# Optimization experiments

Hardware: AMD Instinct MI355X
Metric: run time of the kernel (lower is better)

The kernel has to match this reference:

```python
import jax, jax.numpy as jnp
import numpy as np

D_IN = 4096
D_OUT = 4096
B, S = 4, 2048


def setup_inputs() -> dict:
    key = jax.random.key(0)
    kx, kw, kb = jax.random.split(key, 3)
    x = jax.random.normal(kx, (B, S, D_IN), dtype=jnp.float32)
    # Simulate the quantized weight buffers exactly as QLinear.__init__ does:
    # per-tensor symmetric int8 quantization of a float weight.
    w_fp = jax.random.normal(kw, (D_OUT, D_IN), dtype=jnp.float32) * 0.02
    weight_scale = jnp.max(jnp.abs(w_fp)) / 127.0
    weight_int8 = jnp.round(w_fp / weight_scale).astype(jnp.int8)
    bias = jax.random.normal(kb, (D_OUT,), dtype=jnp.float32) * 0.01
    return {"x": x, "weight_int8": weight_int8, "weight_scale": weight_scale, "bias": bias}


def reference(x, weight_int8, weight_scale, bias):
    # Per-row (last-dim) fake int8 quant-dequant of activations.
    x_scales = jnp.max(jnp.abs(x), axis=-1, keepdims=True) / 127.0 + 1e-8
    xq = jnp.round(x / x_scales) * x_scales
    # Dequantize weight (per-tensor scale) and do the float GEMM.
    w = weight_int8.astype(x.dtype) * weight_scale  # [D_OUT, D_IN]
    y = jnp.einsum("bsd,od->bso", xq, w) + bias
    return y
```

## Files before the change

### kernel.cpp

```cpp
#include <hip/hip_runtime.h>
#include <stdint.h>

#define D_IN  4096
#define D_OUT 4096
#define M_TOT 8192

#define BM 128
#define BN 128
#define BK 64

using i32x4 = __attribute__((ext_vector_type(4))) int;

__global__ __launch_bounds__(256) void prep(
    const float* __restrict__ x, int8_t* __restrict__ xq,
    float* __restrict__ s_out,
    const int* __restrict__ w32, int8_t* __restrict__ w8)
{
    const int tid = threadIdx.x;
    const int b   = blockIdx.x;

    if (b < M_TOT) {
        __shared__ float wmax[4];
        const float* xr = x + (size_t)b * D_IN;

        float4 v[4];
        float m = 0.f;
#pragma unroll
        for (int c = 0; c < 4; ++c) {
            v[c] = ((const float4*)xr)[c * 256 + tid];
            m = fmaxf(m, fmaxf(fmaxf(fabsf(v[c].x), fabsf(v[c].y)),
                               fmaxf(fabsf(v[c].z), fabsf(v[c].w))));
        }
#pragma unroll
        for (int off = 1; off < 64; off <<= 1)
            m = fmaxf(m, __shfl_xor(m, off));
        if ((tid & 63) == 0) wmax[tid >> 6] = m;
        __syncthreads();
        m = fmaxf(fmaxf(wmax[0], wmax[1]), fmaxf(wmax[2], wmax[3]));

        const float s   = m / 127.0f + 1e-8f;
        const float inv = 1.0f / s;
        if (tid == 0) s_out[b] = s;

        int* q32 = (int*)(xq + (size_t)b * D_IN);
#pragma unroll
        for (int c = 0; c < 4; ++c) {
            int q0 = (int)rintf(v[c].x * inv);
            int q1 = (int)rintf(v[c].y * inv);
            int q2 = (int)rintf(v[c].z * inv);
            int q3 = (int)rintf(v[c].w * inv);
            q32[c * 256 + tid] = (q0 & 0xff) | ((q1 & 0xff) << 8) |
                                 ((q2 & 0xff) << 16) | ((q3 & 0xff) << 24);
        }
    } else {
        const int i = (b - M_TOT) * 256 + tid;
        int4 v = ((const int4*)w32)[i];
        ((int*)w8)[i] = (v.x & 0xff) | ((v.y & 0xff) << 8) |
                        ((v.z & 0xff) << 16) | ((v.w & 0xff) << 24);
    }
}

__device__ __forceinline__ void gload_lds16(const void* g, void* l) {
    __builtin_amdgcn_global_load_lds(
        (const __attribute__((address_space(1))) unsigned int*)(uintptr_t)g,
        (__attribute__((address_space(3))) unsigned int*)(uintptr_t)l,
        16, 0, 0);
}

__global__ __launch_bounds__(256) void gemm_i8(
    const int8_t* __restrict__ Aq, const int8_t* __restrict__ Wq,
    const float* __restrict__ srow, const float* __restrict__ wsc,
    const float* __restrict__ bias, float* __restrict__ Y)
{
    __shared__ int8_t lA[BM * BK];
    __shared__ int8_t lB[BN * BK];

    const int tid  = threadIdx.x;
    const int lane = tid & 63;
    const int wave = tid >> 6;

    const int b    = blockIdx.x;
    const int swz  = (b & 7) * 256 + (b >> 3);
    const int nbx  = D_OUT / BN;
    const int bn   = (swz % nbx) * BN;
    const int bm   = (swz / nbx) * BM;

    const int wr   = (wave >> 1) * 64;
    const int wc   = (wave & 1) * 64;

    i32x4 acc[4][4] = {};

    const int fr = lane & 15;
    const int fk = (lane >> 4) * 16;

    const int8_t* gA = Aq + (size_t)bm * D_IN;
    const int8_t* gW = Wq + (size_t)bn * D_IN;

    for (int kt = 0; kt < D_IN; kt += BK) {
#pragma unroll
        for (int j = 0; j < 2; ++j) {
            const int c  = j * 256 + tid;
            const int r  = c >> 2;
            const int ko = (c & 3) * 16;
            gload_lds16(gA + (size_t)r * D_IN + kt + ko, lA + c * 16);
            gload_lds16(gW + (size_t)r * D_IN + kt + ko, lB + c * 16);
        }
        __syncthreads();

        i32x4 a[4], bfr[4];
#pragma unroll
        for (int i = 0; i < 4; ++i) {
            a[i]   = *(const i32x4*)(lA + (wr + i * 16 + fr) * BK + fk);
            bfr[i] = *(const i32x4*)(lB + (wc + i * 16 + fr) * BK + fk);
        }
#pragma unroll
        for (int i = 0; i < 4; ++i)
#pragma unroll
            for (int j = 0; j < 4; ++j)
                acc[i][j] = __builtin_amdgcn_mfma_i32_16x16x64_i8(
                    a[i], bfr[j], acc[i][j], 0, 0, 0);
        __syncthreads();
    }

    const float ws = wsc[0];
    float bs[4];
#pragma unroll
    for (int j = 0; j < 4; ++j) bs[j] = bias[bn + wc + j * 16 + fr];

#pragma unroll
    for (int i = 0; i < 4; ++i) {
        const int m0 = bm + wr + i * 16 + (lane >> 4) * 4;
#pragma unroll
        for (int r = 0; r < 4; ++r) {
            const float sm = srow[m0 + r] * ws;
            float* yp = Y + (size_t)(m0 + r) * D_OUT + bn + wc + fr;
#pragma unroll
            for (int j = 0; j < 4; ++j)
                yp[j * 16] = (float)acc[i][j][r] * sm + bs[j];
        }
    }
}

extern "C" void kernel_launch(void* const* d_in, const int* in_sizes, int n_in,
                              void* d_out, int out_size, void* d_ws, size_t ws_size,
                              hipStream_t stream) {
    const float* x    = (const float*)d_in[0];
    const int*   w32  = (const int*)d_in[1];
    const float* wsc  = (const float*)d_in[2];
    const float* bias = (const float*)d_in[3];
    float* y = (float*)d_out;

    int8_t* xq = (int8_t*)d_ws;
    int8_t* w8 = xq + (size_t)M_TOT * D_IN;
    float*  s  = (float*)(w8 + (size_t)D_OUT * D_IN);

    const int pack_blocks = (D_OUT * D_IN / 4) / 256;
    prep<<<M_TOT + pack_blocks, 256, 0, stream>>>(x, xq, s, w32, w8);

    gemm_i8<<<(M_TOT / BM) * (D_OUT / BN), 256, 0, stream>>>(xq, w8, s, wsc, bias, y);
}
```

Before: 429.5 us.

## Double-buffer LDS tiles in int8 GEMM and drop block swizzle

The int8 GEMM main loop now uses two LDS buffers, so the global-to-LDS load of the next K tile is issued before the MFMAs on the current tile run. The goal is to hide global load latency behind compute and cut one barrier per iteration. It doubles LDS use, which can lower occupancy. It also removes the XCD-aware block index swizzle in favour of plain row-major tile mapping, which may change L2 reuse across chiplets.

```diff
diff --git a/kernel.cpp b/kernel.cpp
--- a/kernel.cpp
+++ b/kernel.cpp
@@ -72,18 +72,15 @@
     const float* __restrict__ srow, const float* __restrict__ wsc,
     const float* __restrict__ bias, float* __restrict__ Y)
 {
-    __shared__ int8_t lA[BM * BK];
-    __shared__ int8_t lB[BN * BK];
+    __shared__ int8_t lA[2][BM * BK];
+    __shared__ int8_t lB[2][BN * BK];
 
     const int tid  = threadIdx.x;
     const int lane = tid & 63;
     const int wave = tid >> 6;
-
-    const int b    = blockIdx.x;
-    const int swz  = (b & 7) * 256 + (b >> 3);
     const int nbx  = D_OUT / BN;
-    const int bn   = (swz % nbx) * BN;
-    const int bm   = (swz / nbx) * BM;
+    const int bn   = ((int)blockIdx.x % nbx) * BN;
+    const int bm   = ((int)blockIdx.x / nbx) * BM;
 
     const int wr   = (wave >> 1) * 64;
     const int wc   = (wave & 1) * 64;
@@ -96,31 +93,49 @@
     const int8_t* gA = Aq + (size_t)bm * D_IN;
     const int8_t* gW = Wq + (size_t)bn * D_IN;
 
-    for (int kt = 0; kt < D_IN; kt += BK) {
-#pragma unroll
-        for (int j = 0; j < 2; ++j) {
-            const int c  = j * 256 + tid;
-            const int r  = c >> 2;
-            const int ko = (c & 3) * 16;
-            gload_lds16(gA + (size_t)r * D_IN + kt + ko, lA + c * 16);
-            gload_lds16(gW + (size_t)r * D_IN + kt + ko, lB + c * 16);
-        }
+#define STAGE(buf, kt)                                                        \
+    {                                                                         \
+        _Pragma("unroll")                                                     \
+        for (int j = 0; j < 2; ++j) {                                         \
+            const int c  = j * 256 + tid;                                     \
+            const int r  = c >> 2;                                            \
+            const int ko = (c & 3) * 16;                                      \
+            gload_lds16(gA + (size_t)r * D_IN + (kt) + ko, &lA[buf][c * 16]); \
+            gload_lds16(gW + (size_t)r * D_IN + (kt) + ko, &lB[buf][c * 16]); \
+        }                                                                     \
+    }
+
+#define COMPUTE(buf)                                                          \
+    {                                                                         \
+        i32x4 a[4], bfr[4];                                                   \
+        _Pragma("unroll")                                                     \
+        for (int i = 0; i < 4; ++i) {                                         \
+            a[i]   = *(const i32x4*)(&lA[buf][(wr + i * 16 + fr) * BK + fk]); \
+            bfr[i] = *(const i32x4*)(&lB[buf][(wc + i * 16 + fr) * BK + fk]); \
+        }                                                                     \
+        _Pragma("unroll")                                                     \
+        for (int i = 0; i < 4; ++i)                                           \
+            _Pragma("unroll")                                                 \
+            for (int j = 0; j < 4; ++j)                                       \
+                acc[i][j] = __builtin_amdgcn_mfma_i32_16x16x64_i8(            \
+                    a[i], bfr[j], acc[i][j], 0, 0, 0);                        \
+    }
+
+    const int NT = D_IN / BK;
+
+    STAGE(0, 0);
+    __syncthreads();
+
+    int cur = 0;
+    for (int t = 0; t < NT - 1; ++t) {
+        STAGE(cur ^ 1, (t + 1) * BK);
+        COMPUTE(cur);
         __syncthreads();
-
-        i32x4 a[4], bfr[4];
-#pragma unroll
-        for (int i = 0; i < 4; ++i) {
-            a[i]   = *(const i32x4*)(lA + (wr + i * 16 + fr) * BK + fk);
-            bfr[i] = *(const i32x4*)(lB + (wc + i * 16 + fr) * BK + fk);
-        }
-#pragma unroll
-        for (int i = 0; i < 4; ++i)
-#pragma unroll
-            for (int j = 0; j < 4; ++j)
-                acc[i][j] = __builtin_amdgcn_mfma_i32_16x16x64_i8(
-                    a[i], bfr[j], acc[i][j], 0, 0, 0);
-        __syncthreads();
+        cur ^= 1;
     }
+    COMPUTE(cur);
+#undef STAGE
+#undef COMPUTE
 
     const float ws = wsc[0];
     float bs[4];
```

New measurement: 427.1 us. No clear change (-0.6%).

## Rewrite int8 GEMM as 256x256 tile with double-buffered LDS pipeline

Applied to the files above, without the earlier changes.

Enlarges the GEMM block tile to 256x256 with K-tiles of 128 and 512 threads, and double-buffers 128KB of LDS so global-to-LDS loads for upcoming K-halves are issued while MFMAs run on the current one. It adds an XOR swizzle on the LDS layout to avoid bank conflicts, explicit vmcnt waits and barriers, and raises wave priority around the MFMA bursts. The goal is to hide memory latency and increase operand reuse per loaded byte. In exchange it uses more registers per thread and the whole LDS, which limits occupancy. It also drops the block-index swizzle used for L2 locality.

```diff
diff --git a/kernel.cpp b/kernel.cpp
--- a/kernel.cpp
+++ b/kernel.cpp
@@ -5,9 +5,10 @@
 #define D_OUT 4096
 #define M_TOT 8192
 
-#define BM 128
-#define BN 128
-#define BK 64
+#define BM 256
+#define BN 256
+#define BKB 128
+#define NT (D_IN / BKB)
 
 using i32x4 = __attribute__((ext_vector_type(4))) int;
 
@@ -67,73 +68,126 @@
         16, 0, 0);
 }
 
-__global__ __launch_bounds__(256) void gemm_i8(
+__global__ __launch_bounds__(512, 2) void gemm_i8(
     const int8_t* __restrict__ Aq, const int8_t* __restrict__ Wq,
     const float* __restrict__ srow, const float* __restrict__ wsc,
     const float* __restrict__ bias, float* __restrict__ Y)
 {
-    __shared__ int8_t lA[BM * BK];
-    __shared__ int8_t lB[BN * BK];
+    __shared__ int8_t lds[131072];
 
     const int tid  = threadIdx.x;
     const int lane = tid & 63;
     const int wave = tid >> 6;
-
-    const int b    = blockIdx.x;
-    const int swz  = (b & 7) * 256 + (b >> 3);
     const int nbx  = D_OUT / BN;
-    const int bn   = (swz % nbx) * BN;
-    const int bm   = (swz / nbx) * BM;
-
-    const int wr   = (wave >> 1) * 64;
-    const int wc   = (wave & 1) * 64;
-
-    i32x4 acc[4][4] = {};
-
-    const int fr = lane & 15;
-    const int fk = (lane >> 4) * 16;
+    const int bn   = ((int)blockIdx.x % nbx) * BN;
+    const int bm   = ((int)blockIdx.x / nbx) * BM;
+    const int wr   = wave >> 2;
+    const int wc   = wave & 3;
+    const int fr   = lane & 15;
+    const int gk   = lane >> 4;
+
+    i32x4 acc[8][4] = {};
 
     const int8_t* gA = Aq + (size_t)bm * D_IN;
-    const int8_t* gW = Wq + (size_t)bn * D_IN;
-
-    for (int kt = 0; kt < D_IN; kt += BK) {
-#pragma unroll
-        for (int j = 0; j < 2; ++j) {
-            const int c  = j * 256 + tid;
-            const int r  = c >> 2;
-            const int ko = (c & 3) * 16;
-            gload_lds16(gA + (size_t)r * D_IN + kt + ko, lA + c * 16);
-            gload_lds16(gW + (size_t)r * D_IN + kt + ko, lB + c * 16);
-        }
-        __syncthreads();
-
-        i32x4 a[4], bfr[4];
-#pragma unroll
-        for (int i = 0; i < 4; ++i) {
-            a[i]   = *(const i32x4*)(lA + (wr + i * 16 + fr) * BK + fk);
-            bfr[i] = *(const i32x4*)(lB + (wc + i * 16 + fr) * BK + fk);
-        }
-#pragma unroll
-        for (int i = 0; i < 4; ++i)
-#pragma unroll
-            for (int j = 0; j < 4; ++j)
-                acc[i][j] = __builtin_amdgcn_mfma_i32_16x16x64_i8(
-                    a[i], bfr[j], acc[i][j], 0, 0, 0);
-        __syncthreads();
-    }
+    const int8_t* gB = Wq + (size_t)bn * D_IN;
+
+#define STAGE_HALF(gbase, kt, kh, lofs)                                        \
+    {                                                                          \
+        _Pragma("unroll")                                                      \
+        for (int u = 0; u < 2; ++u) {                                         \
+            const int c_   = u * 512 + tid;                                   \
+            const int row_ = c_ >> 2;                                         \
+            const int gs_  = (c_ & 3) ^ ((row_ >> 1) & 3);                    \
+            gload_lds16(gbase + (size_t)row_ * D_IN + (kt) + (kh) * 64        \
+                              + gs_ * 16,                                     \
+                        lds + (lofs) + (kh) * 16384 + c_ * 16);               \
+        }                                                                      \
+    }
+
+#define VM8  asm volatile("s_waitcnt vmcnt(8)" ::: "memory")
+#define VM4  asm volatile("s_waitcnt vmcnt(4)" ::: "memory")
+#define VM0  asm volatile("s_waitcnt vmcnt(0)" ::: "memory")
+#define NOWAIT
+#define NOSTAGE
+
+#define PHASE(bufA, bufB, fh, kh, STAGE_STMT, WAIT_STMT)                       \
+    {                                                                          \
+        i32x4 a_[4], b_[4];                                                    \
+        _Pragma("unroll")                                                      \
+        for (int i = 0; i < 4; ++i) {                                         \
+            const int ra_ = wr * 128 + (fh) * 64 + i * 16 + fr;               \
+            a_[i] = *(const i32x4*)(lds + (bufA) + (kh) * 16384 + ra_ * 64    \
+                                    + ((gk ^ ((ra_ >> 1) & 3)) * 16));        \
+            const int rb_ = wc * 64 + i * 16 + fr;                            \
+            b_[i] = *(const i32x4*)(lds + (bufB) + (kh) * 16384 + rb_ * 64    \
+                                    + ((gk ^ ((rb_ >> 1) & 3)) * 16));        \
+        }                                                                      \
+        STAGE_STMT;                                                            \
+        __builtin_amdgcn_s_barrier();                                          \
+        __builtin_amdgcn_s_setprio(1);                                         \
+        _Pragma("unroll")                                                      \
+        for (int i = 0; i < 4; ++i)                                           \
+            _Pragma("unroll")                                                  \
+            for (int j = 0; j < 4; ++j)                                       \
+                acc[(fh) * 4 + i][j] = __builtin_amdgcn_mfma_i32_16x16x64_i8( \
+                    a_[i], b_[j], acc[(fh) * 4 + i][j], 0, 0, 0);             \
+        __builtin_amdgcn_s_setprio(0);                                         \
+        WAIT_STMT;                                                             \
+        __builtin_amdgcn_s_barrier();                                          \
+    }
+
+#define KTILE(buf, S1, S2, S3, S4, W2, W4)                                     \
+    PHASE((buf) * 32768, 65536 + (buf) * 32768, 0, 0, S1, NOWAIT);            \
+    PHASE((buf) * 32768, 65536 + (buf) * 32768, 1, 0, S2, W2);                \
+    PHASE((buf) * 32768, 65536 + (buf) * 32768, 0, 1, S3, NOWAIT);            \
+    PHASE((buf) * 32768, 65536 + (buf) * 32768, 1, 1, S4, W4);
+
+    STAGE_HALF(gA, 0,   0, 0);
+    STAGE_HALF(gB, 0,   0, 65536);
+    STAGE_HALF(gA, 0,   1, 0);
+    STAGE_HALF(gB, 0,   1, 65536);
+    STAGE_HALF(gA, BKB, 0, 32768);
+    STAGE_HALF(gB, BKB, 0, 65536 + 32768);
+    VM4;
+    __builtin_amdgcn_s_barrier();
+
+    for (int t = 0; t < NT - 2; t += 2) {
+        KTILE(0,
+              STAGE_HALF(gA, (t + 1) * BKB, 1, 32768),
+              STAGE_HALF(gB, (t + 1) * BKB, 1, 65536 + 32768),
+              STAGE_HALF(gA, (t + 2) * BKB, 0, 0),
+              STAGE_HALF(gB, (t + 2) * BKB, 0, 65536),
+              VM8, VM8);
+        KTILE(1,
+              STAGE_HALF(gA, (t + 2) * BKB, 1, 0),
+              STAGE_HALF(gB, (t + 2) * BKB, 1, 65536),
+              STAGE_HALF(gA, (t + 3) * BKB, 0, 32768),
+              STAGE_HALF(gB, (t + 3) * BKB, 0, 65536 + 32768),
+              VM8, VM8);
+    }
+    KTILE(0,
+          STAGE_HALF(gA, 31 * BKB, 1, 32768),
+          STAGE_HALF(gB, 31 * BKB, 1, 65536 + 32768),
+          NOSTAGE, NOSTAGE,
+          VM8, VM4);
+    KTILE(1, NOSTAGE, NOSTAGE, NOSTAGE, NOSTAGE, VM0, NOWAIT);
+
+#undef KTILE
+#undef PHASE
+#undef STAGE_HALF
 
     const float ws = wsc[0];
     float bs[4];
 #pragma unroll
-    for (int j = 0; j < 4; ++j) bs[j] = bias[bn + wc + j * 16 + fr];
-
-#pragma unroll
-    for (int i = 0; i < 4; ++i) {
-        const int m0 = bm + wr + i * 16 + (lane >> 4) * 4;
+    for (int j = 0; j < 4; ++j) bs[j] = bias[bn + wc * 64 + j * 16 + fr];
+
+#pragma unroll
+    for (int i = 0; i < 8; ++i) {
+        const int m0 = bm + wr * 128 + i * 16 + gk * 4;
 #pragma unroll
         for (int r = 0; r < 4; ++r) {
             const float sm = srow[m0 + r] * ws;
-            float* yp = Y + (size_t)(m0 + r) * D_OUT + bn + wc + fr;
+            float* yp = Y + (size_t)(m0 + r) * D_OUT + bn + wc * 64 + fr;
 #pragma unroll
             for (int j = 0; j < 4; ++j)
                 yp[j * 16] = (float)acc[i][j][r] * sm + bs[j];
@@ -157,5 +211,5 @@
     const int pack_blocks = (D_OUT * D_IN / 4) / 256;
     prep<<<M_TOT + pack_blocks, 256, 0, stream>>>(x, xq, s, w32, w8);
 
-    gemm_i8<<<(M_TOT / BM) * (D_OUT / BN), 256, 0, stream>>>(xq, w8, s, wsc, bias, y);
-}
+    gemm_i8<<<(M_TOT / BM) * (D_OUT / BN), 512, 0, stream>>>(xq, w8, s, wsc, bias, y);
+}
```

Result: faster. 392.7 us (-8.6%).
